# Kernel tuning notes

Measured on AMD Instinct MI355X. Metric: run time of the kernel, lower is better.

## Reference

```python
import jax, jax.numpy as jnp
import numpy as np

N = 20000   # genes
E = 160000  # directed edges (self-loops added in forward, as PyG GATv2Conv does by default)
D = 64      # input feature dim
H1, C1 = 8, 128  # conv1 heads / channels
LRELU_SLOPE = 0.2
LN_EPS = 1e-5


def setup_inputs() -> dict:
    key = jax.random.key(0)
    ks = jax.random.split(key, 20)
    s = 0.05
    inp = {
        "x": jax.random.normal(ks[0], (N, D), dtype=jnp.float32),
        "edge_index": jax.random.randint(ks[1], (2, E), 0, N, dtype=jnp.int64),
        # conv1 (GATv2Conv D -> H1*C1, concat)
        "Wl1": jax.random.normal(ks[2], (D, H1 * C1), dtype=jnp.float32) * s,
        "bl1": jax.random.normal(ks[3], (H1 * C1,), dtype=jnp.float32) * s,
        "Wr1": jax.random.normal(ks[4], (D, H1 * C1), dtype=jnp.float32) * s,
        "br1": jax.random.normal(ks[5], (H1 * C1,), dtype=jnp.float32) * s,
        "att1": jax.random.normal(ks[6], (H1, C1), dtype=jnp.float32) * s,
        "b1": jax.random.normal(ks[7], (H1 * C1,), dtype=jnp.float32) * s,
        # skip Linear(D -> H1*C1)
        "Wskip": jax.random.normal(ks[8], (D, H1 * C1), dtype=jnp.float32) * s,
        "bskip": jax.random.normal(ks[9], (H1 * C1,), dtype=jnp.float32) * s,
        # LayerNorm(H1*C1)
        "g1": jnp.ones((H1 * C1,), dtype=jnp.float32),
        "beta1": jnp.zeros((H1 * C1,), dtype=jnp.float32),
        # conv2 (GATv2Conv H1*C1 -> 2, heads=1, concat=False)
        "Wl2": jax.random.normal(ks[10], (H1 * C1, 2), dtype=jnp.float32) * s,
        "bl2": jax.random.normal(ks[11], (2,), dtype=jnp.float32) * s,
        "Wr2": jax.random.normal(ks[12], (H1 * C1, 2), dtype=jnp.float32) * s,
        "br2": jax.random.normal(ks[13], (2,), dtype=jnp.float32) * s,
        "att2": jax.random.normal(ks[14], (1, 2), dtype=jnp.float32) * s,
        "b2": jax.random.normal(ks[15], (2,), dtype=jnp.float32) * s,
    }
    return inp


def _gatv2(x, src, dst, Wl, bl, Wr, br, att, bias, heads, ch, concat):
    """PyG GATv2Conv (eval mode): message src -> dst, scatter-softmax over dst."""
    n = x.shape[0]
    xl = (x @ Wl + bl).reshape(n, heads, ch)  # source-side transform
    xr = (x @ Wr + br).reshape(n, heads, ch)  # target-side transform
    e = jax.nn.leaky_relu(xl[src] + xr[dst], LRELU_SLOPE)   # [E,H,C]
    alpha = jnp.einsum('ehc,hc->eh', e, att)                 # [E,H]
    amax = jax.ops.segment_max(alpha, dst, num_segments=n)   # [N,H]
    ex = jnp.exp(alpha - amax[dst])
    denom = jax.ops.segment_sum(ex, dst, num_segments=n)
    alpha = ex / (denom[dst] + 1e-16)
    msg = xl[src] * alpha[..., None]                          # [E,H,C]
    out = jax.ops.segment_sum(msg, dst, num_segments=n)      # [N,H,C]
    out = out.reshape(n, heads * ch) if concat else out.mean(axis=1)
    return out + bias


def _layernorm(x, g, b):
    mu = x.mean(axis=-1, keepdims=True)
    var = ((x - mu) ** 2).mean(axis=-1, keepdims=True)
    return (x - mu) * jax.lax.rsqrt(var + LN_EPS) * g + b


def reference(x, edge_index, Wl1, bl1, Wr1, br1, att1, b1, Wskip, bskip,
              g1, beta1, Wl2, bl2, Wr2, br2, att2, b2):
    n = x.shape[0]
    loop = jnp.arange(n, dtype=edge_index.dtype)  # add_self_loops=True (PyG default)
    src = jnp.concatenate([edge_index[0], loop])
    dst = jnp.concatenate([edge_index[1], loop])
    x1 = _gatv2(x, src, dst, Wl1, bl1, Wr1, br1, att1, b1, H1, C1, True) + (x @ Wskip + bskip)
    x1 = jax.nn.elu(_layernorm(x1, g1, beta1))
    # dropout is a no-op in eval mode
    return _gatv2(x1, src, dst, Wl2, bl2, Wr2, br2, att2, b2, 1, 2, False)
```

## Files before the change

kernel.cpp:

```cpp
#include <hip/hip_runtime.h>
#include <hip/hip_bf16.h>
#include <hip/hip_fp16.h>
#include <math.h>

static constexpr int D  = 64;
static constexpr int F1 = 1024;
static constexpr int NTOT = 3072;

typedef _Float16 f16x8 __attribute__((ext_vector_type(8)));
typedef _Float16 h2    __attribute__((ext_vector_type(2)));
typedef float    f32x4 __attribute__((ext_vector_type(4)));

__device__ __forceinline__ float lrelu(float x) { return x > 0.f ? x : 0.2f * x; }

__device__ __forceinline__ float dot2f(h2 a, h2 b, float c) {
#if __has_builtin(__builtin_amdgcn_fdot2)
    return __builtin_amdgcn_fdot2(a, b, c, false);
#else
    return c + (float)a[0] * (float)b[0] + (float)a[1] * (float)b[1];
#endif
}

__device__ __forceinline__ float red16(float p) {
    int v = __builtin_bit_cast(int, p);
    p += __builtin_bit_cast(float, __builtin_amdgcn_mov_dpp(v, 0xB1, 0xF, 0xF, true));
    v = __builtin_bit_cast(int, p);
    p += __builtin_bit_cast(float, __builtin_amdgcn_mov_dpp(v, 0x4E, 0xF, 0xF, true));
    v = __builtin_bit_cast(int, p);
    p += __builtin_bit_cast(float, __builtin_amdgcn_mov_dpp(v, 0x141, 0xF, 0xF, true));
    v = __builtin_bit_cast(int, p);
    p += __builtin_bit_cast(float, __builtin_amdgcn_mov_dpp(v, 0x140, 0xF, 0xF, true));
    return p;
}

union U4H { uint4 u; h2 h[4]; };

__global__ void k_prep_deg(const float* __restrict__ x,
                           _Float16* __restrict__ xh,
                           const int* __restrict__ ei, int* __restrict__ deg,
                           int n, int ne, int m)
{
    int t = blockIdx.x * blockDim.x + threadIdx.x;
    int ncast = (n * D) / 4;
    if (t < ncast) {
        float4 v = ((const float4*)x)[t];
        union { _Float16 h[4]; uint2 u; } o;
        o.h[0] = (_Float16)v.x; o.h[1] = (_Float16)v.y;
        o.h[2] = (_Float16)v.z; o.h[3] = (_Float16)v.w;
        *(uint2*)(xh + (size_t)t * 4) = o.u;
    }
    if (t < m) {
        int d = (t < ne) ? ei[ne + t] : t - ne;
        atomicAdd(&deg[d], 1);
    }
}

__global__ __launch_bounds__(256) void k_packw(
    const float* __restrict__ Wl1, const float* __restrict__ Wr1,
    const float* __restrict__ Wsk, _Float16* __restrict__ WhT)
{
    __shared__ _Float16 wt[128 * 72];
    const int t = threadIdx.x;
    const int c0 = blockIdx.x * 128;
    const float* __restrict__ W = (c0 < 1024) ? Wl1 : (c0 < 2048) ? Wr1 : Wsk;
    const int cw = c0 & 1023;
#pragma unroll
    for (int q = 0; q < 8; ++q) {
        int idx = t + 256 * q;
        int k = idx >> 5, c4 = (idx & 31) * 4;
        float4 v = *(const float4*)(W + (size_t)k * F1 + cw + c4);
        wt[(c4 + 0) * 72 + k] = (_Float16)v.x;
        wt[(c4 + 1) * 72 + k] = (_Float16)v.y;
        wt[(c4 + 2) * 72 + k] = (_Float16)v.z;
        wt[(c4 + 3) * 72 + k] = (_Float16)v.w;
    }
    __syncthreads();
#pragma unroll
    for (int q = 0; q < 4; ++q) {
        int idx = t + 256 * q;
        int c = idx >> 3, k0 = (idx & 7) * 8;
        uint4 v = *(const uint4*)(&wt[c * 72 + k0]);
        *(uint4*)(WhT + (size_t)(c0 + c) * 64 + k0) = v;
    }
}

__global__ __launch_bounds__(1024) void k_scan(const int* __restrict__ deg,
                                               int* __restrict__ rowptr, int n)
{
    __shared__ int sums[1024];
    const int t = threadIdx.x;
    const int chunk = (n + 1023) / 1024;
    const int base = t * chunk;
    int s = 0;
    for (int i = 0; i < chunk; ++i) {
        int idx = base + i;
        if (idx < n) s += deg[idx];
    }
    sums[t] = s;
    __syncthreads();
    for (int off = 1; off < 1024; off <<= 1) {
        int v = (t >= off) ? sums[t - off] : 0;
        __syncthreads();
        sums[t] += v;
        __syncthreads();
    }
    int run = (t == 0) ? 0 : sums[t - 1];
    for (int i = 0; i < chunk; ++i) {
        int idx = base + i;
        if (idx < n) { rowptr[idx] = run; run += deg[idx]; }
    }
    if (t == 0) rowptr[n] = sums[1023];
}

__global__ void k_scatter(const int* __restrict__ ei, const int* __restrict__ rowptr,
                          int* __restrict__ cursor, int* __restrict__ csr_src,
                          int ne, int m)
{
    int e = blockIdx.x * blockDim.x + threadIdx.x;
    if (e >= m) return;
    int s, d;
    if (e < ne) { s = ei[e]; d = ei[ne + e]; }
    else        { s = e - ne; d = s; }
    int pos = rowptr[d] + atomicAdd(&cursor[d], 1);
    csr_src[pos] = s;
}

#define AS(r, c) smem[(r) * 72 + (c)]
#define BS(r, c) smem[128 * 72 + (r) * 72 + (c)]
#define CS(r, c) smem[(r) * 136 + (c)]
__global__ __launch_bounds__(256) void k_gemm_mfma(
    const _Float16* __restrict__ xh, const _Float16* __restrict__ WhT,
    const float* __restrict__ bl1, const float* __restrict__ br1,
    const float* __restrict__ bsk, const float* __restrict__ b1,
    _Float16* __restrict__ xl1h, _Float16* __restrict__ xr1h,
    _Float16* __restrict__ sk1h, int n)
{
    extern __shared__ _Float16 smem[];
    const int t  = threadIdx.x;
    const int r0 = blockIdx.x * 128;
    const int c0 = blockIdx.y * 128;

#pragma unroll
    for (int q = 0; q < 4; ++q) {
        int c = t + 256 * q;
        int row = c >> 3, off = (c & 7) * 8;
        uint4 v = make_uint4(0, 0, 0, 0);
        if (r0 + row < n) v = *(const uint4*)(xh + (size_t)(r0 + row) * 64 + off);
        *(uint4*)(&AS(row, off)) = v;
        uint4 w = *(const uint4*)(WhT + (size_t)(c0 + row) * 64 + off);
        *(uint4*)(&BS(row, off)) = w;
    }
    __syncthreads();

    const int wave = t >> 6, lane = t & 63;
    const int quad = lane >> 4, l16 = lane & 15;
    const int mw = (wave & 1) * 64, nw = (wave >> 1) * 64;

    f16x8 bfrag[4][2];
#pragma unroll
    for (int nt = 0; nt < 4; ++nt)
#pragma unroll
        for (int ks = 0; ks < 2; ++ks)
            bfrag[nt][ks] = *(const f16x8*)(&BS(nw + nt * 16 + l16, ks * 32 + quad * 8));

    f32x4 acc[4][4];
#pragma unroll
    for (int mt = 0; mt < 4; ++mt)
#pragma unroll
        for (int nt = 0; nt < 4; ++nt) acc[mt][nt] = (f32x4){0.f, 0.f, 0.f, 0.f};

#pragma unroll
    for (int mt = 0; mt < 4; ++mt) {
        f16x8 af[2];
#pragma unroll
        for (int ks = 0; ks < 2; ++ks)
            af[ks] = *(const f16x8*)(&AS(mw + mt * 16 + l16, ks * 32 + quad * 8));
#pragma unroll
        for (int nt = 0; nt < 4; ++nt)
#pragma unroll
            for (int ks = 0; ks < 2; ++ks)
                acc[mt][nt] = __builtin_amdgcn_mfma_f32_16x16x32_f16(
                    af[ks], bfrag[nt][ks], acc[mt][nt], 0, 0, 0);
    }

    const int which = c0 >> 10;
    const int csec  = c0 & 1023;
    __syncthreads();
#pragma unroll
    for (int nt = 0; nt < 4; ++nt) {
        int col = csec + nw + nt * 16 + l16;
        float bias = (which == 0) ? bl1[col] : (which == 1) ? br1[col]
                                             : (bsk[col] + b1[col]);
#pragma unroll
        for (int mt = 0; mt < 4; ++mt) {
#pragma unroll
            for (int r = 0; r < 4; ++r)
                CS(mw + mt * 16 + quad * 4 + r, nw + nt * 16 + l16) =
                    (_Float16)(acc[mt][nt][r] + bias);
        }
    }
    __syncthreads();

    _Float16* __restrict__ dst = (which == 0) ? xl1h : (which == 1) ? xr1h : sk1h;
#pragma unroll
    for (int it = 0; it < 8; ++it) {
        int idx = t + 256 * it;
        int row = idx >> 4, c16 = idx & 15;
        int grow = r0 + row;
        if (grow < n) {
            uint4 v = *(uint4*)(&CS(row, c16 * 8));
            *(uint4*)(dst + (size_t)grow * F1 + csec + c16 * 8) = v;
        }
    }
}

__global__ __launch_bounds__(256, 4) void k_conv1_ln(
    const int* __restrict__ rowptr, const int* __restrict__ csr_src,
    const _Float16* __restrict__ xl1h, const _Float16* __restrict__ xr1h,
    const _Float16* __restrict__ sk1h,
    const float* __restrict__ att1,
    const float* __restrict__ g1, const float* __restrict__ beta1,
    const float* __restrict__ Wl2, const float* __restrict__ bl2,
    const float* __restrict__ Wr2, const float* __restrict__ br2,
    float* __restrict__ xl2, float* __restrict__ xr2, int n)
{
    __shared__ float sb[2][2][6];
    const int slot = threadIdx.x >> 7;
    const int q    = (threadIdx.x >> 6) & 1;
    const int lane = threadIdx.x & 63;
    const int node = blockIdx.x * 2 + slot;
    const bool active = node < n;
    const int cb = q * 512 + lane * 8;
    const h2 c02 = (h2){(_Float16)0.2f, (_Float16)0.2f};

    h2 xr2v[4], at2[4], O[4];
    float ll = 0.f;
    float v[8];
    float s1 = 0.f, s2 = 0.f;

    if (active) {
        U4H u; u.u = *(const uint4*)(xr1h + (size_t)node * F1 + cb);
#pragma unroll
        for (int j = 0; j < 4; ++j) xr2v[j] = u.h[j];
        float4 a0 = *(const float4*)(att1 + cb);
        float4 a1 = *(const float4*)(att1 + cb + 4);
        at2[0] = (h2){(_Float16)a0.x, (_Float16)a0.y};
        at2[1] = (h2){(_Float16)a0.z, (_Float16)a0.w};
        at2[2] = (h2){(_Float16)a1.x, (_Float16)a1.y};
        at2[3] = (h2){(_Float16)a1.z, (_Float16)a1.w};
#pragma unroll
        for (int j = 0; j < 4; ++j) O[j] = (h2){(_Float16)0.f, (_Float16)0.f};

        const int beg = rowptr[node], end = rowptr[node + 1];

        auto edge = [&](const U4H& cur, bool valid) {
            float p = 0.f;
#pragma unroll
            for (int j = 0; j < 4; ++j) {
                h2 s = cur.h[j] + xr2v[j];
                h2 r = __builtin_elementwise_max(s, s * c02);
                p = dot2f(r, at2[j], p);
            }
            p = red16(p);
            float w = valid ? __expf(p) : 0.f;
            ll += w;
            _Float16 wh = (_Float16)w;
            h2 wh2 = (h2){wh, wh};
#pragma unroll
            for (int j = 0; j < 4; ++j) O[j] = O[j] + wh2 * cur.h[j];
        };

        U4H A0, A1, B0, B1;
        {
            int i1 = (beg + 1 < end) ? beg + 1 : beg;
            A0.u = *(const uint4*)(xl1h + (size_t)csr_src[beg] * F1 + cb);
            A1.u = *(const uint4*)(xl1h + (size_t)csr_src[i1]  * F1 + cb);
        }
        int i = beg;
        while (true) {
            bool more = (i + 2 < end);
            if (more) {
                int j0 = i + 2;
                int j1 = (i + 3 < end) ? i + 3 : j0;
                B0.u = *(const uint4*)(xl1h + (size_t)csr_src[j0] * F1 + cb);
                B1.u = *(const uint4*)(xl1h + (size_t)csr_src[j1] * F1 + cb);
            }
            edge(A0, true);
            edge(A1, i + 1 < end);
            i += 2;
            if (!more) break;

            bool more2 = (i + 2 < end);
            if (more2) {
                int j0 = i + 2;
                int j1 = (i + 3 < end) ? i + 3 : j0;
                A0.u = *(const uint4*)(xl1h + (size_t)csr_src[j0] * F1 + cb);
                A1.u = *(const uint4*)(xl1h + (size_t)csr_src[j1] * F1 + cb);
            }
            edge(B0, true);
            edge(B1, i + 1 < end);
            i += 2;
            if (!more2) break;
        }

        float inv = 1.f / (ll + 1e-16f);
        U4H su; su.u = *(const uint4*)(sk1h + (size_t)node * F1 + cb);
#pragma unroll
        for (int j = 0; j < 4; ++j) {
            float xv0 = (float)su.h[j][0] + (float)O[j][0] * inv;
            float xv1 = (float)su.h[j][1] + (float)O[j][1] * inv;
            v[2 * j]     = xv0;
            v[2 * j + 1] = xv1;
            s1 += xv0 + xv1;
            s2 += xv0 * xv0 + xv1 * xv1;
        }
    }
#pragma unroll
    for (int off = 32; off > 0; off >>= 1) {
        s1 += __shfl_xor(s1, off);
        s2 += __shfl_xor(s2, off);
    }
    if (lane == 0) { sb[slot][q][0] = s1; sb[slot][q][1] = s2; }
    __syncthreads();
    float mu  = (sb[slot][0][0] + sb[slot][1][0]) * (1.f / 1024.f);
    float ms  = (sb[slot][0][1] + sb[slot][1][1]) * (1.f / 1024.f);
    float var = fmaxf(ms - mu * mu, 0.f);
    float inv = rsqrtf(var + 1e-5f);

    float p0 = 0.f, p1 = 0.f, p2 = 0.f, p3 = 0.f;
    if (active) {
        float4 gA = *(const float4*)(g1 + cb),    gB = *(const float4*)(g1 + cb + 4);
        float4 bA = *(const float4*)(beta1 + cb), bB = *(const float4*)(beta1 + cb + 4);
        float gv[8] = {gA.x, gA.y, gA.z, gA.w, gB.x, gB.y, gB.z, gB.w};
        float bv[8] = {bA.x, bA.y, bA.z, bA.w, bB.x, bB.y, bB.z, bB.w};
#pragma unroll
        for (int j = 0; j < 8; j += 2) {
            float4 wl = *(const float4*)(Wl2 + (cb + j) * 2);
            float4 wr = *(const float4*)(Wr2 + (cb + j) * 2);
            float y0 = (v[j]   - mu) * inv * gv[j]   + bv[j];
            float y1 = (v[j+1] - mu) * inv * gv[j+1] + bv[j+1];
            float z0 = y0 > 0.f ? y0 : __expf(y0) - 1.f;
            float z1 = y1 > 0.f ? y1 : __expf(y1) - 1.f;
            p0 += z0 * wl.x + z1 * wl.z;
            p1 += z0 * wl.y + z1 * wl.w;
            p2 += z0 * wr.x + z1 * wr.z;
            p3 += z0 * wr.y + z1 * wr.w;
        }
    }
#pragma unroll
    for (int off = 32; off > 0; off >>= 1) {
        p0 += __shfl_xor(p0, off); p1 += __shfl_xor(p1, off);
        p2 += __shfl_xor(p2, off); p3 += __shfl_xor(p3, off);
    }
    if (lane == 0) { sb[slot][q][2] = p0; sb[slot][q][3] = p1;
                     sb[slot][q][4] = p2; sb[slot][q][5] = p3; }
    __syncthreads();
    if (active && lane == 0 && q == 0) {
        xl2[node * 2 + 0] = sb[slot][0][2] + sb[slot][1][2] + bl2[0];
        xl2[node * 2 + 1] = sb[slot][0][3] + sb[slot][1][3] + bl2[1];
        xr2[node * 2 + 0] = sb[slot][0][4] + sb[slot][1][4] + br2[0];
        xr2[node * 2 + 1] = sb[slot][0][5] + sb[slot][1][5] + br2[1];
    }
}

__global__ void k_conv2(const int* __restrict__ rowptr, const int* __restrict__ csr_src,
                        const float* __restrict__ xl2, const float* __restrict__ xr2,
                        const float* __restrict__ att2, const float* __restrict__ b2,
                        float* __restrict__ out2, int n)
{
    int d = blockIdx.x * blockDim.x + threadIdx.x;
    if (d >= n) return;
    float2 xr = *(const float2*)(xr2 + 2 * d);
    float a0w = att2[0], a1w = att2[1];
    float m = -INFINITY, l = 0.f, o0 = 0.f, o1 = 0.f;
    const int beg = rowptr[d], end = rowptr[d + 1];
    float2 pf[2];
    pf[0] = *(const float2*)(xl2 + 2 * csr_src[beg]);
    pf[1] = (beg + 1 < end) ? *(const float2*)(xl2 + 2 * csr_src[beg + 1]) : pf[0];
    for (int i = beg; i < end; ++i) {
        float2 cur = pf[0];
        pf[0] = pf[1];
        if (i + 2 < end) pf[1] = *(const float2*)(xl2 + 2 * csr_src[i + 2]);
        float p = lrelu(cur.x + xr.x) * a0w + lrelu(cur.y + xr.y) * a1w;
        float nm = fmaxf(m, p);
        float sc = __expf(m - nm);
        float w  = __expf(p - nm);
        l = l * sc + w;
        o0 = o0 * sc + w * cur.x;
        o1 = o1 * sc + w * cur.y;
        m = nm;
    }
    float inv = 1.f / (l + 1e-16f);
    out2[2 * d + 0] = o0 * inv + b2[0];
    out2[2 * d + 1] = o1 * inv + b2[1];
}

extern "C" void kernel_launch(void* const* d_in, const int* in_sizes, int n_in,
                              void* d_out, int out_size, void* d_ws, size_t ws_size,
                              hipStream_t stream)
{
    const float* x     = (const float*)d_in[0];
    const int*   ei    = (const int*)  d_in[1];
    const float* Wl1   = (const float*)d_in[2];
    const float* bl1   = (const float*)d_in[3];
    const float* Wr1   = (const float*)d_in[4];
    const float* br1   = (const float*)d_in[5];
    const float* att1  = (const float*)d_in[6];
    const float* b1    = (const float*)d_in[7];
    const float* Wsk   = (const float*)d_in[8];
    const float* bsk   = (const float*)d_in[9];
    const float* g1    = (const float*)d_in[10];
    const float* beta1 = (const float*)d_in[11];
    const float* Wl2   = (const float*)d_in[12];
    const float* bl2   = (const float*)d_in[13];
    const float* Wr2   = (const float*)d_in[14];
    const float* br2   = (const float*)d_in[15];
    const float* att2  = (const float*)d_in[16];
    const float* b2    = (const float*)d_in[17];

    const int n  = in_sizes[0] / D;
    const int ne = in_sizes[1] / 2;
    const int m  = ne + n;

    float* ws = (float*)d_ws;
    size_t o = 0;
    _Float16* xl1h = (_Float16*)(ws + o); o += (size_t)n * F1 / 2;
    _Float16* xr1h = (_Float16*)(ws + o); o += (size_t)n * F1 / 2;
    _Float16* sk1h = (_Float16*)(ws + o); o += (size_t)n * F1 / 2;
    _Float16* xh   = (_Float16*)(ws + o); o += (size_t)n * D / 2;
    _Float16* WhT  = (_Float16*)(ws + o); o += (size_t)NTOT * 64 / 2;
    float* xl2    = ws + o; o += (size_t)n * 2;
    float* xr2    = ws + o; o += (size_t)n * 2;
    int* rowptr   = (int*)(ws + o); o += (size_t)n + 1;
    int* deg      = (int*)(ws + o); o += (size_t)n;
    int* cursor   = (int*)(ws + o); o += (size_t)n;
    int* csr_src  = (int*)(ws + o); o += (size_t)m;
    float* out2   = (float*)d_out;

    hipMemsetAsync(deg, 0, (size_t)2 * n * sizeof(int), stream);
    int prep_threads = (n * D) / 4;
    k_prep_deg<<<(prep_threads + 255) / 256, 256, 0, stream>>>(
        x, xh, ei, deg, n, ne, m);
    k_packw<<<NTOT / 128, 256, 0, stream>>>(Wl1, Wr1, Wsk, WhT);
    k_scan<<<1, 1024, 0, stream>>>(deg, rowptr, n);
    k_scatter<<<(m + 255) / 256, 256, 0, stream>>>(ei, rowptr, cursor, csr_src, ne, m);

    dim3 gg((n + 127) / 128, NTOT / 128);
    k_gemm_mfma<<<gg, 256, 36864, stream>>>(xh, WhT, bl1, br1, bsk, b1,
                                            xl1h, xr1h, sk1h, n);

    k_conv1_ln<<<(n + 1) / 2, 256, 0, stream>>>(rowptr, csr_src, xl1h, xr1h, sk1h,
                                                att1, g1, beta1, Wl2, bl2, Wr2, br2,
                                                xl2, xr2, n);

    k_conv2<<<(n + 255) / 256, 256, 0, stream>>>(rowptr, csr_src, xl2, xr2, att2, b2, out2, n);
}
```

Baseline: 253.1 us.

## Use one 256-thread block per node and precomputed byte offsets in CSR

```diff
diff --git a/kernel.cpp b/kernel.cpp
--- a/kernel.cpp
+++ b/kernel.cpp
@@ -33,7 +33,7 @@
     return p;
 }
 
-union U4H { uint4 u; h2 h[4]; };
+union U2H { uint2 u; h2 h[2]; };
 
 __global__ void k_prep_deg(const float* __restrict__ x,
                            _Float16* __restrict__ xh,
@@ -113,7 +113,7 @@
 }
 
 __global__ void k_scatter(const int* __restrict__ ei, const int* __restrict__ rowptr,
-                          int* __restrict__ cursor, int* __restrict__ csr_src,
+                          int* __restrict__ cursor, int* __restrict__ csr_off,
                           int ne, int m)
 {
     int e = blockIdx.x * blockDim.x + threadIdx.x;
@@ -122,7 +122,7 @@
     if (e < ne) { s = ei[e]; d = ei[ne + e]; }
     else        { s = e - ne; d = s; }
     int pos = rowptr[d] + atomicAdd(&cursor[d], 1);
-    csr_src[pos] = s;
+    csr_off[pos] = s << 11;
 }
 
 #define AS(r, c) smem[(r) * 72 + (c)]
@@ -214,8 +214,8 @@
     }
 }
 
-__global__ __launch_bounds__(256, 4) void k_conv1_ln(
-    const int* __restrict__ rowptr, const int* __restrict__ csr_src,
+__global__ __launch_bounds__(256, 8) void k_conv1_ln(
+    const int* __restrict__ rowptr, const int* __restrict__ csr_off,
     const _Float16* __restrict__ xl1h, const _Float16* __restrict__ xr1h,
     const _Float16* __restrict__ sk1h,
     const float* __restrict__ att1,
@@ -224,57 +224,54 @@
     const float* __restrict__ Wr2, const float* __restrict__ br2,
     float* __restrict__ xl2, float* __restrict__ xr2, int n)
 {
-    __shared__ float sb[2][2][6];
-    const int slot = threadIdx.x >> 7;
-    const int q    = (threadIdx.x >> 6) & 1;
+    __shared__ float sb[4][6];
+    const int qq   = threadIdx.x >> 6;
     const int lane = threadIdx.x & 63;
-    const int node = blockIdx.x * 2 + slot;
-    const bool active = node < n;
-    const int cb = q * 512 + lane * 8;
+    const int node = blockIdx.x;
+    const int cb  = qq * 256 + lane * 4;
+    const int cbB = cb * 2;
     const h2 c02 = (h2){(_Float16)0.2f, (_Float16)0.2f};
-
-    h2 xr2v[4], at2[4], O[4];
+    const char* __restrict__ xlB = (const char*)xl1h;
+
+    h2 xrv[2], at2[2], O[2];
     float ll = 0.f;
-    float v[8];
+    float v[4];
     float s1 = 0.f, s2 = 0.f;
 
-    if (active) {
-        U4H u; u.u = *(const uint4*)(xr1h + (size_t)node * F1 + cb);
-#pragma unroll
-        for (int j = 0; j < 4; ++j) xr2v[j] = u.h[j];
+    {
+        U2H u; u.u = *(const uint2*)(xr1h + (size_t)node * F1 + cb);
+        xrv[0] = u.h[0]; xrv[1] = u.h[1];
         float4 a0 = *(const float4*)(att1 + cb);
-        float4 a1 = *(const float4*)(att1 + cb + 4);
         at2[0] = (h2){(_Float16)a0.x, (_Float16)a0.y};
         at2[1] = (h2){(_Float16)a0.z, (_Float16)a0.w};
-        at2[2] = (h2){(_Float16)a1.x, (_Float16)a1.y};
-        at2[3] = (h2){(_Float16)a1.z, (_Float16)a1.w};
-#pragma unroll
-        for (int j = 0; j < 4; ++j) O[j] = (h2){(_Float16)0.f, (_Float16)0.f};
+        O[0] = (h2){(_Float16)0.f, (_Float16)0.f};
+        O[1] = (h2){(_Float16)0.f, (_Float16)0.f};
 
         const int beg = rowptr[node], end = rowptr[node + 1];
 
-        auto edge = [&](const U4H& cur, bool valid) {
+        auto edge = [&](const U2H& cur, bool valid) {
             float p = 0.f;
 #pragma unroll
-            for (int j = 0; j < 4; ++j) {
-                h2 s = cur.h[j] + xr2v[j];
+            for (int j = 0; j < 2; ++j) {
+                h2 s = cur.h[j] + xrv[j];
                 h2 r = __builtin_elementwise_max(s, s * c02);
                 p = dot2f(r, at2[j], p);
             }
             p = red16(p);
+            p += __shfl_xor(p, 16);
             float w = valid ? __expf(p) : 0.f;
             ll += w;
             _Float16 wh = (_Float16)w;
             h2 wh2 = (h2){wh, wh};
-#pragma unroll
-            for (int j = 0; j < 4; ++j) O[j] = O[j] + wh2 * cur.h[j];
+            O[0] = O[0] + wh2 * cur.h[0];
+            O[1] = O[1] + wh2 * cur.h[1];
         };
 
-        U4H A0, A1, B0, B1;
+        U2H A0, A1, B0, B1;
         {
             int i1 = (beg + 1 < end) ? beg + 1 : beg;
-            A0.u = *(const uint4*)(xl1h + (size_t)csr_src[beg] * F1 + cb);
-            A1.u = *(const uint4*)(xl1h + (size_t)csr_src[i1]  * F1 + cb);
+            A0.u = *(const uint2*)(xlB + (size_t)(unsigned)csr_off[beg] + cbB);
+            A1.u = *(const uint2*)(xlB + (size_t)(unsigned)csr_off[i1]  + cbB);
         }
         int i = beg;
         while (true) {
@@ -282,8 +279,8 @@
             if (more) {
                 int j0 = i + 2;
                 int j1 = (i + 3 < end) ? i + 3 : j0;
-                B0.u = *(const uint4*)(xl1h + (size_t)csr_src[j0] * F1 + cb);
-                B1.u = *(const uint4*)(xl1h + (size_t)csr_src[j1] * F1 + cb);
+                B0.u = *(const uint2*)(xlB + (size_t)(unsigned)csr_off[j0] + cbB);
+                B1.u = *(const uint2*)(xlB + (size_t)(unsigned)csr_off[j1] + cbB);
             }
             edge(A0, true);
             edge(A1, i + 1 < end);
@@ -294,8 +291,8 @@
             if (more2) {
                 int j0 = i + 2;
                 int j1 = (i + 3 < end) ? i + 3 : j0;
-                A0.u = *(const uint4*)(xl1h + (size_t)csr_src[j0] * F1 + cb);
-                A1.u = *(const uint4*)(xl1h + (size_t)csr_src[j1] * F1 + cb);
+                A0.u = *(const uint2*)(xlB + (size_t)(unsigned)csr_off[j0] + cbB);
+                A1.u = *(const uint2*)(xlB + (size_t)(unsigned)csr_off[j1] + cbB);
             }
             edge(B0, true);
             edge(B1, i + 1 < end);
@@ -304,9 +301,9 @@
         }
 
         float inv = 1.f / (ll + 1e-16f);
-        U4H su; su.u = *(const uint4*)(sk1h + (size_t)node * F1 + cb);
-#pragma unroll
-        for (int j = 0; j < 4; ++j) {
+        U2H su; su.u = *(const uint2*)(sk1h + (size_t)node * F1 + cb);
+#pragma unroll
+        for (int j = 0; j < 2; ++j) {
             float xv0 = (float)su.h[j][0] + (float)O[j][0] * inv;
             float xv1 = (float)su.h[j][1] + (float)O[j][1] * inv;
             v[2 * j]     = xv0;
@@ -320,50 +317,51 @@
         s1 += __shfl_xor(s1, off);
         s2 += __shfl_xor(s2, off);
     }
-    if (lane == 0) { sb[slot][q][0] = s1; sb[slot][q][1] = s2; }
-    __syncthreads();
-    float mu  = (sb[slot][0][0] + sb[slot][1][0]) * (1.f / 1024.f);
-    float ms  = (sb[slot][0][1] + sb[slot][1][1]) * (1.f / 1024.f);
+    if (lane == 0) { sb[qq][0] = s1; sb[qq][1] = s2; }
+    __syncthreads();
+    float mu  = (sb[0][0] + sb[1][0] + sb[2][0] + sb[3][0]) * (1.f / 1024.f);
+    float ms  = (sb[0][1] + sb[1][1] + sb[2][1] + sb[3][1]) * (1.f / 1024.f);
     float var = fmaxf(ms - mu * mu, 0.f);
     float inv = rsqrtf(var + 1e-5f);
 
-    float p0 = 0.f, p1 = 0.f, p2 = 0.f, p3 = 0.f;
-    if (active) {
-        float4 gA = *(const float4*)(g1 + cb),    gB = *(const float4*)(g1 + cb + 4);
-        float4 bA = *(const float4*)(beta1 + cb), bB = *(const float4*)(beta1 + cb + 4);
-        float gv[8] = {gA.x, gA.y, gA.z, gA.w, gB.x, gB.y, gB.z, gB.w};
-        float bv[8] = {bA.x, bA.y, bA.z, bA.w, bB.x, bB.y, bB.z, bB.w};
-#pragma unroll
-        for (int j = 0; j < 8; j += 2) {
-            float4 wl = *(const float4*)(Wl2 + (cb + j) * 2);
-            float4 wr = *(const float4*)(Wr2 + (cb + j) * 2);
-            float y0 = (v[j]   - mu) * inv * gv[j]   + bv[j];
-            float y1 = (v[j+1] - mu) * inv * gv[j+1] + bv[j+1];
-            float z0 = y0 > 0.f ? y0 : __expf(y0) - 1.f;
-            float z1 = y1 > 0.f ? y1 : __expf(y1) - 1.f;
-            p0 += z0 * wl.x + z1 * wl.z;
-            p1 += z0 * wl.y + z1 * wl.w;
-            p2 += z0 * wr.x + z1 * wr.z;
-            p3 += z0 * wr.y + z1 * wr.w;
-        }
+    float p0, p1, p2, p3;
+    {
+        float4 gA = *(const float4*)(g1 + cb);
+        float4 bA = *(const float4*)(beta1 + cb);
+        float gv[4] = {gA.x, gA.y, gA.z, gA.w};
+        float bv[4] = {bA.x, bA.y, bA.z, bA.w};
+        float z[4];
+#pragma unroll
+        for (int j = 0; j < 4; ++j) {
+            float y = (v[j] - mu) * inv * gv[j] + bv[j];
+            z[j] = y > 0.f ? y : __expf(y) - 1.f;
+        }
+        float4 wl0 = *(const float4*)(Wl2 + cb * 2);
+        float4 wl1 = *(const float4*)(Wl2 + cb * 2 + 4);
+        float4 wr0 = *(const float4*)(Wr2 + cb * 2);
+        float4 wr1 = *(const float4*)(Wr2 + cb * 2 + 4);
+        p0 = z[0] * wl0.x + z[1] * wl0.z + z[2] * wl1.x + z[3] * wl1.z;
+        p1 = z[0] * wl0.y + z[1] * wl0.w + z[2] * wl1.y + z[3] * wl1.w;
+        p2 = z[0] * wr0.x + z[1] * wr0.z + z[2] * wr1.x + z[3] * wr1.z;
+        p3 = z[0] * wr0.y + z[1] * wr0.w + z[2] * wr1.y + z[3] * wr1.w;
     }
 #pragma unroll
     for (int off = 32; off > 0; off >>= 1) {
         p0 += __shfl_xor(p0, off); p1 += __shfl_xor(p1, off);
         p2 += __shfl_xor(p2, off); p3 += __shfl_xor(p3, off);
     }
-    if (lane == 0) { sb[slot][q][2] = p0; sb[slot][q][3] = p1;
-                     sb[slot][q][4] = p2; sb[slot][q][5] = p3; }
-    __syncthreads();
-    if (active && lane == 0 && q == 0) {
-        xl2[node * 2 + 0] = sb[slot][0][2] + sb[slot][1][2] + bl2[0];
-        xl2[node * 2 + 1] = sb[slot][0][3] + sb[slot][1][3] + bl2[1];
-        xr2[node * 2 + 0] = sb[slot][0][4] + sb[slot][1][4] + br2[0];
-        xr2[node * 2 + 1] = sb[slot][0][5] + sb[slot][1][5] + br2[1];
-    }
-}
-
-__global__ void k_conv2(const int* __restrict__ rowptr, const int* __restrict__ csr_src,
+    if (lane == 0) { sb[qq][2] = p0; sb[qq][3] = p1;
+                     sb[qq][4] = p2; sb[qq][5] = p3; }
+    __syncthreads();
+    if (threadIdx.x == 0) {
+        xl2[node * 2 + 0] = sb[0][2] + sb[1][2] + sb[2][2] + sb[3][2] + bl2[0];
+        xl2[node * 2 + 1] = sb[0][3] + sb[1][3] + sb[2][3] + sb[3][3] + bl2[1];
+        xr2[node * 2 + 0] = sb[0][4] + sb[1][4] + sb[2][4] + sb[3][4] + br2[0];
+        xr2[node * 2 + 1] = sb[0][5] + sb[1][5] + sb[2][5] + sb[3][5] + br2[1];
+    }
+}
+
+__global__ void k_conv2(const int* __restrict__ rowptr, const int* __restrict__ csr_off,
                         const float* __restrict__ xl2, const float* __restrict__ xr2,
                         const float* __restrict__ att2, const float* __restrict__ b2,
                         float* __restrict__ out2, int n)
@@ -375,12 +373,12 @@
     float m = -INFINITY, l = 0.f, o0 = 0.f, o1 = 0.f;
     const int beg = rowptr[d], end = rowptr[d + 1];
     float2 pf[2];
-    pf[0] = *(const float2*)(xl2 + 2 * csr_src[beg]);
-    pf[1] = (beg + 1 < end) ? *(const float2*)(xl2 + 2 * csr_src[beg + 1]) : pf[0];
+    pf[0] = *(const float2*)(xl2 + 2 * (csr_off[beg] >> 11));
+    pf[1] = (beg + 1 < end) ? *(const float2*)(xl2 + 2 * (csr_off[beg + 1] >> 11)) : pf[0];
     for (int i = beg; i < end; ++i) {
         float2 cur = pf[0];
         pf[0] = pf[1];
-        if (i + 2 < end) pf[1] = *(const float2*)(xl2 + 2 * csr_src[i + 2]);
+        if (i + 2 < end) pf[1] = *(const float2*)(xl2 + 2 * (csr_off[i + 2] >> 11));
         float p = lrelu(cur.x + xr.x) * a0w + lrelu(cur.y + xr.y) * a1w;
         float nm = fmaxf(m, p);
         float sc = __expf(m - nm);
@@ -434,7 +432,7 @@
     int* rowptr   = (int*)(ws + o); o += (size_t)n + 1;
     int* deg      = (int*)(ws + o); o += (size_t)n;
     int* cursor   = (int*)(ws + o); o += (size_t)n;
-    int* csr_src  = (int*)(ws + o); o += (size_t)m;
+    int* csr_off  = (int*)(ws + o); o += (size_t)m;
     float* out2   = (float*)d_out;
 
     hipMemsetAsync(deg, 0, (size_t)2 * n * sizeof(int), stream);
@@ -443,15 +441,15 @@
         x, xh, ei, deg, n, ne, m);
     k_packw<<<NTOT / 128, 256, 0, stream>>>(Wl1, Wr1, Wsk, WhT);
     k_scan<<<1, 1024, 0, stream>>>(deg, rowptr, n);
-    k_scatter<<<(m + 255) / 256, 256, 0, stream>>>(ei, rowptr, cursor, csr_src, ne, m);
+    k_scatter<<<(m + 255) / 256, 256, 0, stream>>>(ei, rowptr, cursor, csr_off, ne, m);
 
     dim3 gg((n + 127) / 128, NTOT / 128);
     k_gemm_mfma<<<gg, 256, 36864, stream>>>(xh, WhT, bl1, br1, bsk, b1,
                                             xl1h, xr1h, sk1h, n);
 
-    k_conv1_ln<<<(n + 1) / 2, 256, 0, stream>>>(rowptr, csr_src, xl1h, xr1h, sk1h,
-                                                att1, g1, beta1, Wl2, bl2, Wr2, br2,
-                                                xl2, xr2, n);
-
-    k_conv2<<<(n + 255) / 256, 256, 0, stream>>>(rowptr, csr_src, xl2, xr2, att2, b2, out2, n);
-}
+    k_conv1_ln<<<n, 256, 0, stream>>>(rowptr, csr_off, xl1h, xr1h, sk1h,
+                                      att1, g1, beta1, Wl2, bl2, Wr2, br2,
+                                      xl2, xr2, n);
+
+    k_conv2<<<(n + 255) / 256, 256, 0, stream>>>(rowptr, csr_off, xl2, xr2, att2, b2, out2, n);
+}
```

After: 253.5 us. No clear change (+0.2%).
